# Performance work log

Hardware: AMD Instinct MI355X
Metric: run time of the kernel (lower is better)

The kernel has to match this reference:

```python
import jax, jax.numpy as jnp
import numpy as np

N_NODES = 100000
N_EDGES = 3200000
D_IN = 256
D_OUT = 256


def setup_inputs() -> dict:
    key = jax.random.key(0)
    k1, k2, k3, k4, k5 = jax.random.split(key, 5)
    x = jax.random.normal(k1, (N_NODES, D_IN), dtype=jnp.float32)
    edge_row = jax.random.randint(k2, (N_EDGES,), 0, N_NODES, dtype=jnp.int32)
    edge_col = jax.random.randint(k3, (N_EDGES,), 0, N_NODES, dtype=jnp.int32)
    edge_val = jax.random.uniform(k4, (N_EDGES,), dtype=jnp.float32)
    # Linear weight [out_dim, in_dim], kaiming-uniform-like scale
    bound = 1.0 / np.sqrt(D_IN)
    W = jax.random.uniform(k5, (D_OUT, D_IN), dtype=jnp.float32,
                           minval=-bound, maxval=bound)
    return {"x": x, "edge_row": edge_row, "edge_col": edge_col,
            "edge_val": edge_val, "W": W}


def reference(x, edge_row, edge_col, edge_val, W):
    # SpMM: agg[i] = sum_{edges e with row=i} val_e * x[col_e]
    msgs = edge_val[:, None] * x[edge_col]            # [E, D_IN] gather
    agg = jax.ops.segment_sum(msgs, edge_row, num_segments=N_NODES)  # [N, D_IN]
    # Dense linear projection (bias=False): agg @ W.T
    return agg @ W.T                                  # [N, D_OUT]
```

## Files before the change

kernel.cpp:

```cpp
#include <hip/hip_runtime.h>
#include <stdint.h>

#define N_NODES 100000
#define N_EDGES 3200000
#define D_FEAT 256
#define NBKT 391
#define CHUNK 8192
#define NBLK_E 391

typedef __attribute__((ext_vector_type(8))) short short8;
typedef __attribute__((ext_vector_type(8))) ushort ushort8;
typedef __attribute__((ext_vector_type(4))) float float4v;

__device__ inline unsigned short f2bf(float f) {
    union { float f; unsigned u; } v; v.f = f;
    unsigned u = v.u;
    u += 0x7FFF + ((u >> 16) & 1);
    return (unsigned short)(u >> 16);
}
__device__ inline float bf2f(unsigned short u) {
    union { unsigned u; float f; } v; v.u = (unsigned)u << 16;
    return v.f;
}

__global__ void wconv_kernel(const float* __restrict__ W, ushort* __restrict__ Wbf) {
    int i = blockIdx.x * 256 + threadIdx.x;
    Wbf[i] = f2bf(W[i]);
}

__global__ __launch_bounds__(256) void gemm_x_kernel(
        const float* __restrict__ x,
        const ushort* __restrict__ Wbf,
        ushort* __restrict__ ybf) {
    int w    = threadIdx.x >> 6;
    int lane = threadIdx.x & 63;
    int quad = lane >> 4;
    int l16  = lane & 15;
    int rt   = blockIdx.x * 64;

    float4v acc[4][4];
    #pragma unroll
    for (int mt = 0; mt < 4; ++mt)
        #pragma unroll
        for (int nt = 0; nt < 4; ++nt) acc[mt][nt] = (float4v){0.f, 0.f, 0.f, 0.f};

    #pragma unroll
    for (int k0 = 0; k0 < 256; k0 += 32) {
        short8 a[4], bf[4];
        #pragma unroll
        for (int mt = 0; mt < 4; ++mt) {
            int row = rt + mt * 16 + l16;
            if (row >= N_NODES) row = N_NODES - 1;
            const float4v* p = (const float4v*)&x[(size_t)row * 256 + k0 + quad * 8];
            float4v f0 = p[0], f1 = p[1];
            a[mt][0] = (short)f2bf(f0.x); a[mt][1] = (short)f2bf(f0.y);
            a[mt][2] = (short)f2bf(f0.z); a[mt][3] = (short)f2bf(f0.w);
            a[mt][4] = (short)f2bf(f1.x); a[mt][5] = (short)f2bf(f1.y);
            a[mt][6] = (short)f2bf(f1.z); a[mt][7] = (short)f2bf(f1.w);
        }
        #pragma unroll
        for (int nt = 0; nt < 4; ++nt) {
            int n = w * 64 + nt * 16 + l16;
            bf[nt] = *(const short8*)&Wbf[n * 256 + k0 + quad * 8];
        }
        #pragma unroll
        for (int mt = 0; mt < 4; ++mt)
            #pragma unroll
            for (int nt = 0; nt < 4; ++nt)
                acc[mt][nt] = __builtin_amdgcn_mfma_f32_16x16x32_bf16(a[mt], bf[nt], acc[mt][nt], 0, 0, 0);
    }
    #pragma unroll
    for (int mt = 0; mt < 4; ++mt)
        #pragma unroll
        for (int nt = 0; nt < 4; ++nt) {
            int n = w * 64 + nt * 16 + l16;
            #pragma unroll
            for (int r = 0; r < 4; ++r) {
                int row = rt + mt * 16 + quad * 4 + r;
                if (row < N_NODES) ybf[(size_t)row * 256 + n] = f2bf(acc[mt][nt][r]);
            }
        }
}

__global__ __launch_bounds__(256) void coarse_hist(const int* __restrict__ key,
                                                   int* __restrict__ hist) {
    __shared__ int cnt[NBKT];
    for (int b = threadIdx.x; b < NBKT; b += 256) cnt[b] = 0;
    __syncthreads();
    int cb = blockIdx.x * CHUNK;
    for (int j = 0; j < CHUNK; j += 256) {
        int i = cb + j + threadIdx.x;
        if (i < N_EDGES) atomicAdd(&cnt[key[i] >> 8], 1);
    }
    __syncthreads();
    for (int b = threadIdx.x; b < NBKT; b += 256)
        hist[blockIdx.x * NBKT + b] = cnt[b];
}

__global__ __launch_bounds__(512) void scan_blocks(int* __restrict__ hist,
                                                   int* __restrict__ totals) {
    __shared__ int s[512];
    int b = blockIdx.x;
    int t = threadIdx.x;
    int v = (t < NBLK_E) ? hist[t * NBKT + b] : 0;
    s[t] = v;
    __syncthreads();
    for (int o = 1; o < 512; o <<= 1) {
        int x = (t >= o) ? s[t - o] : 0;
        __syncthreads();
        s[t] += x;
        __syncthreads();
    }
    if (t < NBLK_E) hist[t * NBKT + b] = s[t] - v;
    if (t == NBLK_E - 1) totals[b] = s[t];
}

__global__ __launch_bounds__(512) void scan_buckets(const int* __restrict__ totals,
                                                    int* __restrict__ base_,
                                                    int* __restrict__ row_start) {
    __shared__ int s[512];
    int t = threadIdx.x;
    int v = (t < NBKT) ? totals[t] : 0;
    s[t] = v;
    __syncthreads();
    for (int o = 1; o < 512; o <<= 1) {
        int x = (t >= o) ? s[t - o] : 0;
        __syncthreads();
        s[t] += x;
        __syncthreads();
    }
    if (t < NBKT) base_[t] = s[t] - v;
    if (t == 0) { base_[NBKT] = N_EDGES; row_start[N_NODES] = N_EDGES; }
}

__global__ __launch_bounds__(256) void col_scatter(
        const int* __restrict__ erow, const int* __restrict__ ecol,
        const float* __restrict__ eval,
        const int* __restrict__ hist, const int* __restrict__ base_,
        int* __restrict__ tmpr, uint2* __restrict__ tmpcv) {
    __shared__ int lbase[NBKT];
    __shared__ int cnt[NBKT];
    for (int b = threadIdx.x; b < NBKT; b += 256) {
        lbase[b] = hist[blockIdx.x * NBKT + b] + base_[b];
        cnt[b] = 0;
    }
    __syncthreads();
    int cb = blockIdx.x * CHUNK;
    for (int j = 0; j < CHUNK; j += 256) {
        int i = cb + j + threadIdx.x;
        if (i < N_EDGES) {
            int c = ecol[i];
            int r = erow[i];
            int b = c >> 8;
            int pos = lbase[b] + atomicAdd(&cnt[b], 1);
            tmpr[pos] = r;
            uint2 cv;
            cv.x = (unsigned)c | ((unsigned)(r & 255) << 17);
            union { float f; unsigned u; } w; w.f = eval[i];
            cv.y = w.u;
            tmpcv[pos] = cv;
        }
    }
}

__global__ __launch_bounds__(256) void row_scatter(
        const int* __restrict__ tmpr, const uint2* __restrict__ tmpcv,
        const int* __restrict__ hist, const int* __restrict__ base_,
        uint2* __restrict__ tmp) {
    __shared__ int lbase[NBKT];
    __shared__ int cnt[NBKT];
    for (int b = threadIdx.x; b < NBKT; b += 256) {
        lbase[b] = hist[blockIdx.x * NBKT + b] + base_[b];
        cnt[b] = 0;
    }
    __syncthreads();
    int cb = blockIdx.x * CHUNK;
    for (int j = 0; j < CHUNK; j += 256) {
        int i = cb + j + threadIdx.x;
        if (i < N_EDGES) {
            int b = tmpr[i] >> 8;
            int pos = lbase[b] + atomicAdd(&cnt[b], 1);
            tmp[pos] = tmpcv[i];
        }
    }
}

__global__ __launch_bounds__(256) void fine_sort(const uint2* __restrict__ tmp,
                                                 const int* __restrict__ base_,
                                                 uint2* __restrict__ csr,
                                                 int* __restrict__ row_start) {
    __shared__ int cnt[256];
    __shared__ int excl[256];
    int b = blockIdx.x;
    int t = threadIdx.x;
    int s0 = base_[b];
    int nb = base_[b + 1] - s0;
    cnt[t] = 0;
    __syncthreads();
    for (int j = t; j < nb; j += 256)
        atomicAdd(&cnt[tmp[s0 + j].x >> 17], 1);
    __syncthreads();
    int v = cnt[t];
    excl[t] = v;
    __syncthreads();
    for (int o = 1; o < 256; o <<= 1) {
        int x = (t >= o) ? excl[t - o] : 0;
        __syncthreads();
        excl[t] += x;
        __syncthreads();
    }
    int ex = excl[t] - v;
    int row = b * 256 + t;
    if (row < N_NODES) row_start[row] = s0 + ex;
    excl[t] = ex;
    cnt[t] = 0;
    __syncthreads();
    for (int j = t; j < nb; j += 256) {
        uint2 cv = tmp[s0 + j];
        unsigned rl = cv.x >> 17;
        int dst = s0 + excl[rl] + atomicAdd(&cnt[rl], 1);
        csr[dst] = cv;
    }
}

__global__ __launch_bounds__(256) void spmm_kernel(
        const ushort* __restrict__ ybf,
        const int* __restrict__ row_start,
        const uint2* __restrict__ csr_cv,
        float* __restrict__ out) {
    int row  = (blockIdx.x * blockDim.x + threadIdx.x) >> 6;
    int lane = threadIdx.x & 63;
    int half = lane >> 5;
    int hl   = lane & 31;
    if (row >= N_NODES) return;
    int start = row_start[row];
    int end   = row_start[row + 1];
    float acc[8] = {0.f, 0.f, 0.f, 0.f, 0.f, 0.f, 0.f, 0.f};
    int e = start + half;
    for (; e + 6 < end; e += 8) {
        uint2 cv0 = csr_cv[e];
        uint2 cv1 = csr_cv[e + 2];
        uint2 cv2 = csr_cv[e + 4];
        uint2 cv3 = csr_cv[e + 6];
        ushort8 v0 = *(const ushort8*)&ybf[(size_t)(cv0.x & 0x1FFFF) * 256 + hl * 8];
        ushort8 v1 = *(const ushort8*)&ybf[(size_t)(cv1.x & 0x1FFFF) * 256 + hl * 8];
        ushort8 v2 = *(const ushort8*)&ybf[(size_t)(cv2.x & 0x1FFFF) * 256 + hl * 8];
        ushort8 v3 = *(const ushort8*)&ybf[(size_t)(cv3.x & 0x1FFFF) * 256 + hl * 8];
        union { unsigned u; float f; } w0, w1, w2, w3;
        w0.u = cv0.y; w1.u = cv1.y; w2.u = cv2.y; w3.u = cv3.y;
        #pragma unroll
        for (int j = 0; j < 8; ++j) acc[j] += w0.f * bf2f(v0[j]);
        #pragma unroll
        for (int j = 0; j < 8; ++j) acc[j] += w1.f * bf2f(v1[j]);
        #pragma unroll
        for (int j = 0; j < 8; ++j) acc[j] += w2.f * bf2f(v2[j]);
        #pragma unroll
        for (int j = 0; j < 8; ++j) acc[j] += w3.f * bf2f(v3[j]);
    }
    for (; e < end; e += 2) {
        uint2 cv = csr_cv[e];
        ushort8 v = *(const ushort8*)&ybf[(size_t)(cv.x & 0x1FFFF) * 256 + hl * 8];
        union { unsigned u; float f; } w; w.u = cv.y;
        #pragma unroll
        for (int j = 0; j < 8; ++j) acc[j] += w.f * bf2f(v[j]);
    }
    #pragma unroll
    for (int j = 0; j < 8; ++j) acc[j] += __shfl_xor(acc[j], 32, 64);
    if (half == 0) {
        float4v o0 = {acc[0], acc[1], acc[2], acc[3]};
        float4v o1 = {acc[4], acc[5], acc[6], acc[7]};
        *(float4v*)&out[(size_t)row * 256 + hl * 8]     = o0;
        *(float4v*)&out[(size_t)row * 256 + hl * 8 + 4] = o1;
    }
}


extern "C" void kernel_launch(void* const* d_in, const int* in_sizes, int n_in,
                              void* d_out, int out_size, void* d_ws, size_t ws_size,
                              hipStream_t stream) {
    const float* x    = (const float*)d_in[0];
    const int*   erow = (const int*)d_in[1];
    const int*   ecol = (const int*)d_in[2];
    const float* eval = (const float*)d_in[3];
    const float* W    = (const float*)d_in[4];
    float* out = (float*)d_out;

    char* ws = (char*)d_ws;
    size_t off = 0;
    int* hist      = (int*)(ws + off);   off += ((size_t)NBLK_E * NBKT * 4 + 255) & ~255ull;
    int* totals    = (int*)(ws + off);   off += ((size_t)NBKT * 4 + 255) & ~255ull;
    int* base_     = (int*)(ws + off);   off += ((size_t)(NBKT + 1) * 4 + 255) & ~255ull;
    int* row_start = (int*)(ws + off);   off += ((size_t)(N_NODES + 1) * 4 + 255) & ~255ull;
    int* tmpr      = (int*)(ws + off);   off += ((size_t)N_EDGES * 4 + 255) & ~255ull;
    uint2* tmpcv   = (uint2*)(ws + off); off += (size_t)N_EDGES * 8;
    uint2* tmp_cv  = (uint2*)(ws + off); off += (size_t)N_EDGES * 8;
    uint2* csr_cv  = (uint2*)(ws + off); off += (size_t)N_EDGES * 8;
    ushort* Wbf    = (ushort*)(ws + off);  off += (size_t)D_FEAT * D_FEAT * 2;
    ushort* ybf    = (ushort*)(ws + off);  off += (size_t)N_NODES * D_FEAT * 2;

    wconv_kernel<<<(D_FEAT * D_FEAT) / 256, 256, 0, stream>>>(W, Wbf);
    gemm_x_kernel<<<(N_NODES + 63) / 64, 256, 0, stream>>>(x, Wbf, ybf);

    coarse_hist<<<NBLK_E, 256, 0, stream>>>(ecol, hist);
    scan_blocks<<<NBKT, 512, 0, stream>>>(hist, totals);
    scan_buckets<<<1, 512, 0, stream>>>(totals, base_, row_start);
    col_scatter<<<NBLK_E, 256, 0, stream>>>(erow, ecol, eval, hist, base_, tmpr, tmpcv);
    coarse_hist<<<NBLK_E, 256, 0, stream>>>(tmpr, hist);
    scan_blocks<<<NBKT, 512, 0, stream>>>(hist, totals);
    scan_buckets<<<1, 512, 0, stream>>>(totals, base_, row_start);
    row_scatter<<<NBLK_E, 256, 0, stream>>>(tmpr, tmpcv, hist, base_, tmp_cv);
    fine_sort<<<NBKT, 256, 0, stream>>>(tmp_cv, base_, csr_cv, row_start);

    spmm_kernel<<<N_NODES / 4, 256, 0, stream>>>(ybf, row_start, csr_cv, out);
}
```

Baseline: 701.7 us.

## Replace two-pass radix CSR build with global-atomic row counting and scatter

Drops the column-then-row two-pass bucket sort, with its temporaries and fine-sort pass. It builds the CSR directly: per-row edge counts are taken with global atomics fused into the GEMM kernel, then a two-level scan and a single atomic-cursor scatter follow. This removes several launches and about two full passes over the edge arrays. The catch is that order within a row becomes nondeterministic and the column sort is gone, so gathers from ybf lose locality and global atomics may contend.

```diff
diff --git a/kernel.cpp b/kernel.cpp
--- a/kernel.cpp
+++ b/kernel.cpp
@@ -4,9 +4,8 @@
 #define N_NODES 100000
 #define N_EDGES 3200000
 #define D_FEAT 256
-#define NBKT 391
-#define CHUNK 8192
-#define NBLK_E 391
+#define NROWBLK 391
+#define EPB 2048
 
 typedef __attribute__((ext_vector_type(8))) short short8;
 typedef __attribute__((ext_vector_type(8))) ushort ushort8;
@@ -23,15 +22,32 @@
     return v.f;
 }
 
-__global__ void wconv_kernel(const float* __restrict__ W, ushort* __restrict__ Wbf) {
-    int i = blockIdx.x * 256 + threadIdx.x;
-    Wbf[i] = f2bf(W[i]);
+__global__ __launch_bounds__(256) void prep_kernel(const float* __restrict__ W,
+                                                   ushort* __restrict__ Wbf,
+                                                   int* __restrict__ row_cnt) {
+    int b = blockIdx.x;
+    if (b < 256) {
+        int i = b * 256 + threadIdx.x;
+        Wbf[i] = f2bf(W[i]);
+    } else {
+        int i = (b - 256) * 256 + threadIdx.x;
+        if (i < N_NODES) row_cnt[i] = 0;
+    }
 }
 
 __global__ __launch_bounds__(256) void gemm_x_kernel(
         const float* __restrict__ x,
         const ushort* __restrict__ Wbf,
+        const int* __restrict__ erow,
+        int* __restrict__ row_cnt,
         ushort* __restrict__ ybf) {
+    int eb = blockIdx.x * EPB;
+    #pragma unroll
+    for (int j = 0; j < EPB; j += 256) {
+        int i = eb + j + threadIdx.x;
+        if (i < N_EDGES) atomicAdd(&row_cnt[erow[i]], 1);
+    }
+
     int w    = threadIdx.x >> 6;
     int lane = threadIdx.x & 63;
     int quad = lane >> 4;
@@ -82,37 +98,23 @@
         }
 }
 
-__global__ __launch_bounds__(256) void coarse_hist(const int* __restrict__ key,
-                                                   int* __restrict__ hist) {
-    __shared__ int cnt[NBKT];
-    for (int b = threadIdx.x; b < NBKT; b += 256) cnt[b] = 0;
+__global__ __launch_bounds__(256) void scan_rows(const int* __restrict__ row_cnt,
+                                                 int* __restrict__ row_start,
+                                                 int* __restrict__ totals) {
+    __shared__ int s[256];
+    int b = blockIdx.x, t = threadIdx.x;
+    int row = b * 256 + t;
+    int c = (row < N_NODES) ? row_cnt[row] : 0;
+    s[t] = c;
     __syncthreads();
-    int cb = blockIdx.x * CHUNK;
-    for (int j = 0; j < CHUNK; j += 256) {
-        int i = cb + j + threadIdx.x;
-        if (i < N_EDGES) atomicAdd(&cnt[key[i] >> 8], 1);
-    }
-    __syncthreads();
-    for (int b = threadIdx.x; b < NBKT; b += 256)
-        hist[blockIdx.x * NBKT + b] = cnt[b];
-}
-
-__global__ __launch_bounds__(512) void scan_blocks(int* __restrict__ hist,
-                                                   int* __restrict__ totals) {
-    __shared__ int s[512];
-    int b = blockIdx.x;
-    int t = threadIdx.x;
-    int v = (t < NBLK_E) ? hist[t * NBKT + b] : 0;
-    s[t] = v;
-    __syncthreads();
-    for (int o = 1; o < 512; o <<= 1) {
+    for (int o = 1; o < 256; o <<= 1) {
         int x = (t >= o) ? s[t - o] : 0;
         __syncthreads();
         s[t] += x;
         __syncthreads();
     }
-    if (t < NBLK_E) hist[t * NBKT + b] = s[t] - v;
-    if (t == NBLK_E - 1) totals[b] = s[t];
+    if (row < N_NODES) row_start[row] = s[t] - c;
+    if (t == 255) totals[b] = s[t];
 }
 
 __global__ __launch_bounds__(512) void scan_buckets(const int* __restrict__ totals,
@@ -120,7 +122,7 @@
                                                     int* __restrict__ row_start) {
     __shared__ int s[512];
     int t = threadIdx.x;
-    int v = (t < NBKT) ? totals[t] : 0;
+    int v = (t < NROWBLK) ? totals[t] : 0;
     s[t] = v;
     __syncthreads();
     for (int o = 1; o < 512; o <<= 1) {
@@ -129,98 +131,33 @@
         s[t] += x;
         __syncthreads();
     }
-    if (t < NBKT) base_[t] = s[t] - v;
-    if (t == 0) { base_[NBKT] = N_EDGES; row_start[N_NODES] = N_EDGES; }
-}
-
-__global__ __launch_bounds__(256) void col_scatter(
+    if (t < NROWBLK) base_[t] = s[t] - v;
+    if (t == 0) row_start[N_NODES] = N_EDGES;
+}
+
+__global__ __launch_bounds__(256) void finalize_rows(int* __restrict__ row_start,
+                                                     const int* __restrict__ base_,
+                                                     int* __restrict__ cursor) {
+    int i = blockIdx.x * 256 + threadIdx.x;
+    if (i < N_NODES) {
+        int v = row_start[i] + base_[i >> 8];
+        row_start[i] = v;
+        cursor[i] = v;
+    }
+}
+
+__global__ __launch_bounds__(256) void scatter_kernel(
         const int* __restrict__ erow, const int* __restrict__ ecol,
         const float* __restrict__ eval,
-        const int* __restrict__ hist, const int* __restrict__ base_,
-        int* __restrict__ tmpr, uint2* __restrict__ tmpcv) {
-    __shared__ int lbase[NBKT];
-    __shared__ int cnt[NBKT];
-    for (int b = threadIdx.x; b < NBKT; b += 256) {
-        lbase[b] = hist[blockIdx.x * NBKT + b] + base_[b];
-        cnt[b] = 0;
-    }
-    __syncthreads();
-    int cb = blockIdx.x * CHUNK;
-    for (int j = 0; j < CHUNK; j += 256) {
-        int i = cb + j + threadIdx.x;
-        if (i < N_EDGES) {
-            int c = ecol[i];
-            int r = erow[i];
-            int b = c >> 8;
-            int pos = lbase[b] + atomicAdd(&cnt[b], 1);
-            tmpr[pos] = r;
-            uint2 cv;
-            cv.x = (unsigned)c | ((unsigned)(r & 255) << 17);
-            union { float f; unsigned u; } w; w.f = eval[i];
-            cv.y = w.u;
-            tmpcv[pos] = cv;
-        }
-    }
-}
-
-__global__ __launch_bounds__(256) void row_scatter(
-        const int* __restrict__ tmpr, const uint2* __restrict__ tmpcv,
-        const int* __restrict__ hist, const int* __restrict__ base_,
-        uint2* __restrict__ tmp) {
-    __shared__ int lbase[NBKT];
-    __shared__ int cnt[NBKT];
-    for (int b = threadIdx.x; b < NBKT; b += 256) {
-        lbase[b] = hist[blockIdx.x * NBKT + b] + base_[b];
-        cnt[b] = 0;
-    }
-    __syncthreads();
-    int cb = blockIdx.x * CHUNK;
-    for (int j = 0; j < CHUNK; j += 256) {
-        int i = cb + j + threadIdx.x;
-        if (i < N_EDGES) {
-            int b = tmpr[i] >> 8;
-            int pos = lbase[b] + atomicAdd(&cnt[b], 1);
-            tmp[pos] = tmpcv[i];
-        }
-    }
-}
-
-__global__ __launch_bounds__(256) void fine_sort(const uint2* __restrict__ tmp,
-                                                 const int* __restrict__ base_,
-                                                 uint2* __restrict__ csr,
-                                                 int* __restrict__ row_start) {
-    __shared__ int cnt[256];
-    __shared__ int excl[256];
-    int b = blockIdx.x;
-    int t = threadIdx.x;
-    int s0 = base_[b];
-    int nb = base_[b + 1] - s0;
-    cnt[t] = 0;
-    __syncthreads();
-    for (int j = t; j < nb; j += 256)
-        atomicAdd(&cnt[tmp[s0 + j].x >> 17], 1);
-    __syncthreads();
-    int v = cnt[t];
-    excl[t] = v;
-    __syncthreads();
-    for (int o = 1; o < 256; o <<= 1) {
-        int x = (t >= o) ? excl[t - o] : 0;
-        __syncthreads();
-        excl[t] += x;
-        __syncthreads();
-    }
-    int ex = excl[t] - v;
-    int row = b * 256 + t;
-    if (row < N_NODES) row_start[row] = s0 + ex;
-    excl[t] = ex;
-    cnt[t] = 0;
-    __syncthreads();
-    for (int j = t; j < nb; j += 256) {
-        uint2 cv = tmp[s0 + j];
-        unsigned rl = cv.x >> 17;
-        int dst = s0 + excl[rl] + atomicAdd(&cnt[rl], 1);
-        csr[dst] = cv;
-    }
+        int* __restrict__ cursor, uint2* __restrict__ csr) {
+    int i = blockIdx.x * 256 + threadIdx.x;
+    int r = erow[i];
+    int dst = atomicAdd(&cursor[r], 1);
+    uint2 cv;
+    cv.x = (unsigned)ecol[i];
+    union { float f; unsigned u; } w; w.f = eval[i];
+    cv.y = w.u;
+    csr[dst] = cv;
 }
 
 __global__ __launch_bounds__(256) void spmm_kernel(
@@ -242,10 +179,10 @@
         uint2 cv1 = csr_cv[e + 2];
         uint2 cv2 = csr_cv[e + 4];
         uint2 cv3 = csr_cv[e + 6];
-        ushort8 v0 = *(const ushort8*)&ybf[(size_t)(cv0.x & 0x1FFFF) * 256 + hl * 8];
-        ushort8 v1 = *(const ushort8*)&ybf[(size_t)(cv1.x & 0x1FFFF) * 256 + hl * 8];
-        ushort8 v2 = *(const ushort8*)&ybf[(size_t)(cv2.x & 0x1FFFF) * 256 + hl * 8];
-        ushort8 v3 = *(const ushort8*)&ybf[(size_t)(cv3.x & 0x1FFFF) * 256 + hl * 8];
+        ushort8 v0 = *(const ushort8*)&ybf[(size_t)cv0.x * 256 + hl * 8];
+        ushort8 v1 = *(const ushort8*)&ybf[(size_t)cv1.x * 256 + hl * 8];
+        ushort8 v2 = *(const ushort8*)&ybf[(size_t)cv2.x * 256 + hl * 8];
+        ushort8 v3 = *(const ushort8*)&ybf[(size_t)cv3.x * 256 + hl * 8];
         union { unsigned u; float f; } w0, w1, w2, w3;
         w0.u = cv0.y; w1.u = cv1.y; w2.u = cv2.y; w3.u = cv3.y;
         #pragma unroll
@@ -259,7 +196,7 @@
     }
     for (; e < end; e += 2) {
         uint2 cv = csr_cv[e];
-        ushort8 v = *(const ushort8*)&ybf[(size_t)(cv.x & 0x1FFFF) * 256 + hl * 8];
+        ushort8 v = *(const ushort8*)&ybf[(size_t)cv.x * 256 + hl * 8];
         union { unsigned u; float f; } w; w.u = cv.y;
         #pragma unroll
         for (int j = 0; j < 8; ++j) acc[j] += w.f * bf2f(v[j]);
@@ -287,29 +224,20 @@
 
     char* ws = (char*)d_ws;
     size_t off = 0;
-    int* hist      = (int*)(ws + off);   off += ((size_t)NBLK_E * NBKT * 4 + 255) & ~255ull;
-    int* totals    = (int*)(ws + off);   off += ((size_t)NBKT * 4 + 255) & ~255ull;
-    int* base_     = (int*)(ws + off);   off += ((size_t)(NBKT + 1) * 4 + 255) & ~255ull;
+    int* row_cnt   = (int*)(ws + off);   off += ((size_t)N_NODES * 4 + 255) & ~255ull;
     int* row_start = (int*)(ws + off);   off += ((size_t)(N_NODES + 1) * 4 + 255) & ~255ull;
-    int* tmpr      = (int*)(ws + off);   off += ((size_t)N_EDGES * 4 + 255) & ~255ull;
-    uint2* tmpcv   = (uint2*)(ws + off); off += (size_t)N_EDGES * 8;
-    uint2* tmp_cv  = (uint2*)(ws + off); off += (size_t)N_EDGES * 8;
+    int* cursor    = (int*)(ws + off);   off += ((size_t)N_NODES * 4 + 255) & ~255ull;
+    int* totals    = (int*)(ws + off);   off += ((size_t)NROWBLK * 4 + 255) & ~255ull;
+    int* base_     = (int*)(ws + off);   off += ((size_t)NROWBLK * 4 + 255) & ~255ull;
     uint2* csr_cv  = (uint2*)(ws + off); off += (size_t)N_EDGES * 8;
     ushort* Wbf    = (ushort*)(ws + off);  off += (size_t)D_FEAT * D_FEAT * 2;
     ushort* ybf    = (ushort*)(ws + off);  off += (size_t)N_NODES * D_FEAT * 2;
 
-    wconv_kernel<<<(D_FEAT * D_FEAT) / 256, 256, 0, stream>>>(W, Wbf);
-    gemm_x_kernel<<<(N_NODES + 63) / 64, 256, 0, stream>>>(x, Wbf, ybf);
-
-    coarse_hist<<<NBLK_E, 256, 0, stream>>>(ecol, hist);
-    scan_blocks<<<NBKT, 512, 0, stream>>>(hist, totals);
+    prep_kernel<<<256 + NROWBLK, 256, 0, stream>>>(W, Wbf, row_cnt);
+    gemm_x_kernel<<<(N_NODES + 63) / 64, 256, 0, stream>>>(x, Wbf, erow, row_cnt, ybf);
+    scan_rows<<<NROWBLK, 256, 0, stream>>>(row_cnt, row_start, totals);
     scan_buckets<<<1, 512, 0, stream>>>(totals, base_, row_start);
-    col_scatter<<<NBLK_E, 256, 0, stream>>>(erow, ecol, eval, hist, base_, tmpr, tmpcv);
-    coarse_hist<<<NBLK_E, 256, 0, stream>>>(tmpr, hist);
-    scan_blocks<<<NBKT, 512, 0, stream>>>(hist, totals);
-    scan_buckets<<<1, 512, 0, stream>>>(totals, base_, row_start);
-    row_scatter<<<NBLK_E, 256, 0, stream>>>(tmpr, tmpcv, hist, base_, tmp_cv);
-    fine_sort<<<NBKT, 256, 0, stream>>>(tmp_cv, base_, csr_cv, row_start);
-
+    finalize_rows<<<NROWBLK, 256, 0, stream>>>(row_start, base_, cursor);
+    scatter_kernel<<<N_EDGES / 256, 256, 0, stream>>>(erow, ecol, eval, cursor, csr_cv);
     spmm_kernel<<<N_NODES / 4, 256, 0, stream>>>(ybf, row_start, csr_cv, out);
 }
```

After: 828.3 us. 1.18x slower.

## Replace column-then-row bucket sort with two-level row radix partitioning

Applied to the files above, without the earlier changes.

The sort pipeline changes from a column-bucket pass followed by a row-bucket pass to an MSD-style two-level partition on the row key. The first level uses 25 coarse buckets (row>>12), the second uses 391 buckets (row>>8). The intermediate row key is stored as a 16-bit value instead of a 32-bit int, which cuts scatter traffic. Edges within a row are no longer pre-ordered by column, so x-row gather locality in the SpMM may drop. The coarse first scatter with only 25 buckets also risks more contention on the shared-memory atomics.

```diff
diff --git a/kernel.cpp b/kernel.cpp
--- a/kernel.cpp
+++ b/kernel.cpp
@@ -4,9 +4,10 @@
 #define N_NODES 100000
 #define N_EDGES 3200000
 #define D_FEAT 256
-#define NBKT 391
 #define CHUNK 8192
 #define NBLK_E 391
+#define NB1 25
+#define NB2 391
 
 typedef __attribute__((ext_vector_type(8))) short short8;
 typedef __attribute__((ext_vector_type(8))) ushort ushort8;
@@ -82,27 +83,42 @@
         }
 }
 
-__global__ __launch_bounds__(256) void coarse_hist(const int* __restrict__ key,
-                                                   int* __restrict__ hist) {
-    __shared__ int cnt[NBKT];
-    for (int b = threadIdx.x; b < NBKT; b += 256) cnt[b] = 0;
+__global__ __launch_bounds__(256) void hist1_kernel(const int* __restrict__ erow,
+                                                    int* __restrict__ hist) {
+    __shared__ int cnt[NB1];
+    if (threadIdx.x < NB1) cnt[threadIdx.x] = 0;
     __syncthreads();
     int cb = blockIdx.x * CHUNK;
     for (int j = 0; j < CHUNK; j += 256) {
         int i = cb + j + threadIdx.x;
-        if (i < N_EDGES) atomicAdd(&cnt[key[i] >> 8], 1);
-    }
-    __syncthreads();
-    for (int b = threadIdx.x; b < NBKT; b += 256)
-        hist[blockIdx.x * NBKT + b] = cnt[b];
+        if (i < N_EDGES) atomicAdd(&cnt[erow[i] >> 12], 1);
+    }
+    __syncthreads();
+    if (threadIdx.x < NB1) hist[blockIdx.x * NB1 + threadIdx.x] = cnt[threadIdx.x];
+}
+
+__global__ __launch_bounds__(256) void hist2_kernel(const ushort* __restrict__ rh1,
+                                                    int* __restrict__ hist) {
+    __shared__ int cnt[NB2];
+    for (int b = threadIdx.x; b < NB2; b += 256) cnt[b] = 0;
+    __syncthreads();
+    int cb = blockIdx.x * CHUNK;
+    for (int j = 0; j < CHUNK; j += 256) {
+        int i = cb + j + threadIdx.x;
+        if (i < N_EDGES) atomicAdd(&cnt[rh1[i]], 1);
+    }
+    __syncthreads();
+    for (int b = threadIdx.x; b < NB2; b += 256)
+        hist[blockIdx.x * NB2 + b] = cnt[b];
 }
 
 __global__ __launch_bounds__(512) void scan_blocks(int* __restrict__ hist,
-                                                   int* __restrict__ totals) {
+                                                   int* __restrict__ totals,
+                                                   int nbkt) {
     __shared__ int s[512];
     int b = blockIdx.x;
     int t = threadIdx.x;
-    int v = (t < NBLK_E) ? hist[t * NBKT + b] : 0;
+    int v = (t < NBLK_E) ? hist[t * nbkt + b] : 0;
     s[t] = v;
     __syncthreads();
     for (int o = 1; o < 512; o <<= 1) {
@@ -111,16 +127,16 @@
         s[t] += x;
         __syncthreads();
     }
-    if (t < NBLK_E) hist[t * NBKT + b] = s[t] - v;
+    if (t < NBLK_E) hist[t * nbkt + b] = s[t] - v;
     if (t == NBLK_E - 1) totals[b] = s[t];
 }
 
 __global__ __launch_bounds__(512) void scan_buckets(const int* __restrict__ totals,
                                                     int* __restrict__ base_,
-                                                    int* __restrict__ row_start) {
+                                                    int n, int* __restrict__ row_start) {
     __shared__ int s[512];
     int t = threadIdx.x;
-    int v = (t < NBKT) ? totals[t] : 0;
+    int v = (t < n) ? totals[t] : 0;
     s[t] = v;
     __syncthreads();
     for (int o = 1; o < 512; o <<= 1) {
@@ -129,19 +145,51 @@
         s[t] += x;
         __syncthreads();
     }
-    if (t < NBKT) base_[t] = s[t] - v;
-    if (t == 0) { base_[NBKT] = N_EDGES; row_start[N_NODES] = N_EDGES; }
-}
-
-__global__ __launch_bounds__(256) void col_scatter(
+    if (t < n) base_[t] = s[t] - v;
+    if (t == 0) {
+        base_[n] = N_EDGES;
+        if (row_start) row_start[N_NODES] = N_EDGES;
+    }
+}
+
+__global__ __launch_bounds__(256) void scatter1_kernel(
         const int* __restrict__ erow, const int* __restrict__ ecol,
         const float* __restrict__ eval,
-        const int* __restrict__ hist, const int* __restrict__ base_,
-        int* __restrict__ tmpr, uint2* __restrict__ tmpcv) {
-    __shared__ int lbase[NBKT];
-    __shared__ int cnt[NBKT];
-    for (int b = threadIdx.x; b < NBKT; b += 256) {
-        lbase[b] = hist[blockIdx.x * NBKT + b] + base_[b];
+        const int* __restrict__ hist1, const int* __restrict__ base1,
+        ushort* __restrict__ rh1, uint2* __restrict__ cv1) {
+    __shared__ int lbase[NB1];
+    __shared__ int cnt[NB1];
+    int t = threadIdx.x;
+    if (t < NB1) {
+        lbase[t] = hist1[blockIdx.x * NB1 + t] + base1[t];
+        cnt[t] = 0;
+    }
+    __syncthreads();
+    int cb = blockIdx.x * CHUNK;
+    for (int j = 0; j < CHUNK; j += 256) {
+        int i = cb + j + t;
+        if (i < N_EDGES) {
+            int r = erow[i];
+            int b = r >> 12;
+            int pos = lbase[b] + atomicAdd(&cnt[b], 1);
+            rh1[pos] = (unsigned short)(r >> 8);
+            uint2 cv;
+            cv.x = (unsigned)ecol[i] | ((unsigned)(r & 255) << 17);
+            union { float f; unsigned u; } w; w.f = eval[i];
+            cv.y = w.u;
+            cv1[pos] = cv;
+        }
+    }
+}
+
+__global__ __launch_bounds__(256) void scatter2_kernel(
+        const ushort* __restrict__ rh1, const uint2* __restrict__ cv1,
+        const int* __restrict__ hist2, const int* __restrict__ base2,
+        uint2* __restrict__ tmp2) {
+    __shared__ int lbase[NB2];
+    __shared__ int cnt[NB2];
+    for (int b = threadIdx.x; b < NB2; b += 256) {
+        lbase[b] = hist2[blockIdx.x * NB2 + b] + base2[b];
         cnt[b] = 0;
     }
     __syncthreads();
@@ -149,38 +197,9 @@
     for (int j = 0; j < CHUNK; j += 256) {
         int i = cb + j + threadIdx.x;
         if (i < N_EDGES) {
-            int c = ecol[i];
-            int r = erow[i];
-            int b = c >> 8;
+            int b = rh1[i];
             int pos = lbase[b] + atomicAdd(&cnt[b], 1);
-            tmpr[pos] = r;
-            uint2 cv;
-            cv.x = (unsigned)c | ((unsigned)(r & 255) << 17);
-            union { float f; unsigned u; } w; w.f = eval[i];
-            cv.y = w.u;
-            tmpcv[pos] = cv;
-        }
-    }
-}
-
-__global__ __launch_bounds__(256) void row_scatter(
-        const int* __restrict__ tmpr, const uint2* __restrict__ tmpcv,
-        const int* __restrict__ hist, const int* __restrict__ base_,
-        uint2* __restrict__ tmp) {
-    __shared__ int lbase[NBKT];
-    __shared__ int cnt[NBKT];
-    for (int b = threadIdx.x; b < NBKT; b += 256) {
-        lbase[b] = hist[blockIdx.x * NBKT + b] + base_[b];
-        cnt[b] = 0;
-    }
-    __syncthreads();
-    int cb = blockIdx.x * CHUNK;
-    for (int j = 0; j < CHUNK; j += 256) {
-        int i = cb + j + threadIdx.x;
-        if (i < N_EDGES) {
-            int b = tmpr[i] >> 8;
-            int pos = lbase[b] + atomicAdd(&cnt[b], 1);
-            tmp[pos] = tmpcv[i];
+            tmp2[pos] = cv1[i];
         }
     }
 }
@@ -287,29 +306,32 @@
 
     char* ws = (char*)d_ws;
     size_t off = 0;
-    int* hist      = (int*)(ws + off);   off += ((size_t)NBLK_E * NBKT * 4 + 255) & ~255ull;
-    int* totals    = (int*)(ws + off);   off += ((size_t)NBKT * 4 + 255) & ~255ull;
-    int* base_     = (int*)(ws + off);   off += ((size_t)(NBKT + 1) * 4 + 255) & ~255ull;
+    int* hist1     = (int*)(ws + off);   off += ((size_t)NBLK_E * NB1 * 4 + 255) & ~255ull;
+    int* hist2     = (int*)(ws + off);   off += ((size_t)NBLK_E * NB2 * 4 + 255) & ~255ull;
+    int* totals1   = (int*)(ws + off);   off += (512 * 4);
+    int* base1     = (int*)(ws + off);   off += (512 * 4);
+    int* totals2   = (int*)(ws + off);   off += (512 * 4);
+    int* base2     = (int*)(ws + off);   off += (512 * 4);
     int* row_start = (int*)(ws + off);   off += ((size_t)(N_NODES + 1) * 4 + 255) & ~255ull;
-    int* tmpr      = (int*)(ws + off);   off += ((size_t)N_EDGES * 4 + 255) & ~255ull;
-    uint2* tmpcv   = (uint2*)(ws + off); off += (size_t)N_EDGES * 8;
-    uint2* tmp_cv  = (uint2*)(ws + off); off += (size_t)N_EDGES * 8;
-    uint2* csr_cv  = (uint2*)(ws + off); off += (size_t)N_EDGES * 8;
-    ushort* Wbf    = (ushort*)(ws + off);  off += (size_t)D_FEAT * D_FEAT * 2;
-    ushort* ybf    = (ushort*)(ws + off);  off += (size_t)N_NODES * D_FEAT * 2;
+    ushort* rh1    = (ushort*)(ws + off); off += ((size_t)N_EDGES * 2 + 255) & ~255ull;
+    uint2* cv1     = (uint2*)(ws + off);  off += (size_t)N_EDGES * 8;
+    uint2* tmp2    = (uint2*)(ws + off);  off += (size_t)N_EDGES * 8;
+    uint2* csr_cv  = (uint2*)(ws + off);  off += (size_t)N_EDGES * 8;
+    ushort* Wbf    = (ushort*)(ws + off); off += (size_t)D_FEAT * D_FEAT * 2;
+    ushort* ybf    = (ushort*)(ws + off); off += (size_t)N_NODES * D_FEAT * 2;
 
     wconv_kernel<<<(D_FEAT * D_FEAT) / 256, 256, 0, stream>>>(W, Wbf);
     gemm_x_kernel<<<(N_NODES + 63) / 64, 256, 0, stream>>>(x, Wbf, ybf);
 
-    coarse_hist<<<NBLK_E, 256, 0, stream>>>(ecol, hist);
-    scan_blocks<<<NBKT, 512, 0, stream>>>(hist, totals);
-    scan_buckets<<<1, 512, 0, stream>>>(totals, base_, row_start);
-    col_scatter<<<NBLK_E, 256, 0, stream>>>(erow, ecol, eval, hist, base_, tmpr, tmpcv);
-    coarse_hist<<<NBLK_E, 256, 0, stream>>>(tmpr, hist);
-    scan_blocks<<<NBKT, 512, 0, stream>>>(hist, totals);
-    scan_buckets<<<1, 512, 0, stream>>>(totals, base_, row_start);
-    row_scatter<<<NBLK_E, 256, 0, stream>>>(tmpr, tmpcv, hist, base_, tmp_cv);
-    fine_sort<<<NBKT, 256, 0, stream>>>(tmp_cv, base_, csr_cv, row_start);
+    hist1_kernel<<<NBLK_E, 256, 0, stream>>>(erow, hist1);
+    scan_blocks<<<NB1, 512, 0, stream>>>(hist1, totals1, NB1);
+    scan_buckets<<<1, 512, 0, stream>>>(totals1, base1, NB1, nullptr);
+    scatter1_kernel<<<NBLK_E, 256, 0, stream>>>(erow, ecol, eval, hist1, base1, rh1, cv1);
+    hist2_kernel<<<NBLK_E, 256, 0, stream>>>(rh1, hist2);
+    scan_blocks<<<NB2, 512, 0, stream>>>(hist2, totals2, NB2);
+    scan_buckets<<<1, 512, 0, stream>>>(totals2, base2, NB2, row_start);
+    scatter2_kernel<<<NBLK_E, 256, 0, stream>>>(rh1, cv1, hist2, base2, tmp2);
+    fine_sort<<<NB2, 256, 0, stream>>>(tmp2, base2, csr_cv, row_start);
 
     spmm_kernel<<<N_NODES / 4, 256, 0, stream>>>(ybf, row_start, csr_cv, out);
 }
```

Measured after the change: 615.4 us. 1.14x faster.

## Drop column pre-sort pass; bucket edges by row directly with wider blocks

Applied to the files above, without the earlier changes.

Removes the first sort pass that ordered edges by column bucket, along with its histogram, scans and temporary arrays. Edges now go straight into row buckets in a single scatter, then the fine sort runs as before. Histogram and scatter blocks grow to 1024 threads and fine_sort to 512 threads. Within each row the edges lose their column-sorted order, so gathers in the SpMM may have worse cache locality, and the fine sort's atomic order makes summation order nondeterministic.

```diff
diff --git a/kernel.cpp b/kernel.cpp
--- a/kernel.cpp
+++ b/kernel.cpp
@@ -4,9 +4,10 @@
 #define N_NODES 100000
 #define N_EDGES 3200000
 #define D_FEAT 256
-#define NBKT 391
 #define CHUNK 8192
 #define NBLK_E 391
+#define NBKT 391
+#define CT 1024
 
 typedef __attribute__((ext_vector_type(8))) short short8;
 typedef __attribute__((ext_vector_type(8))) ushort ushort8;
@@ -82,19 +83,19 @@
         }
 }
 
-__global__ __launch_bounds__(256) void coarse_hist(const int* __restrict__ key,
-                                                   int* __restrict__ hist) {
+__global__ __launch_bounds__(CT) void hist_kernel(const int* __restrict__ erow,
+                                                  int* __restrict__ hist) {
     __shared__ int cnt[NBKT];
-    for (int b = threadIdx.x; b < NBKT; b += 256) cnt[b] = 0;
+    if (threadIdx.x < NBKT) cnt[threadIdx.x] = 0;
     __syncthreads();
     int cb = blockIdx.x * CHUNK;
-    for (int j = 0; j < CHUNK; j += 256) {
+    #pragma unroll
+    for (int j = 0; j < CHUNK; j += CT) {
         int i = cb + j + threadIdx.x;
-        if (i < N_EDGES) atomicAdd(&cnt[key[i] >> 8], 1);
-    }
-    __syncthreads();
-    for (int b = threadIdx.x; b < NBKT; b += 256)
-        hist[blockIdx.x * NBKT + b] = cnt[b];
+        if (i < N_EDGES) atomicAdd(&cnt[erow[i] >> 8], 1);
+    }
+    __syncthreads();
+    if (threadIdx.x < NBKT) hist[blockIdx.x * NBKT + threadIdx.x] = cnt[threadIdx.x];
 }
 
 __global__ __launch_bounds__(512) void scan_blocks(int* __restrict__ hist,
@@ -133,59 +134,37 @@
     if (t == 0) { base_[NBKT] = N_EDGES; row_start[N_NODES] = N_EDGES; }
 }
 
-__global__ __launch_bounds__(256) void col_scatter(
+__global__ __launch_bounds__(CT) void scatter_kernel(
         const int* __restrict__ erow, const int* __restrict__ ecol,
         const float* __restrict__ eval,
-        const int* __restrict__ hist, const int* __restrict__ base_,
-        int* __restrict__ tmpr, uint2* __restrict__ tmpcv) {
-    __shared__ int lbase[NBKT];
-    __shared__ int cnt[NBKT];
-    for (int b = threadIdx.x; b < NBKT; b += 256) {
-        lbase[b] = hist[blockIdx.x * NBKT + b] + base_[b];
-        cnt[b] = 0;
-    }
-    __syncthreads();
-    int cb = blockIdx.x * CHUNK;
-    for (int j = 0; j < CHUNK; j += 256) {
-        int i = cb + j + threadIdx.x;
-        if (i < N_EDGES) {
-            int c = ecol[i];
-            int r = erow[i];
-            int b = c >> 8;
-            int pos = lbase[b] + atomicAdd(&cnt[b], 1);
-            tmpr[pos] = r;
-            uint2 cv;
-            cv.x = (unsigned)c | ((unsigned)(r & 255) << 17);
-            union { float f; unsigned u; } w; w.f = eval[i];
-            cv.y = w.u;
-            tmpcv[pos] = cv;
-        }
-    }
-}
-
-__global__ __launch_bounds__(256) void row_scatter(
-        const int* __restrict__ tmpr, const uint2* __restrict__ tmpcv,
         const int* __restrict__ hist, const int* __restrict__ base_,
         uint2* __restrict__ tmp) {
     __shared__ int lbase[NBKT];
     __shared__ int cnt[NBKT];
-    for (int b = threadIdx.x; b < NBKT; b += 256) {
-        lbase[b] = hist[blockIdx.x * NBKT + b] + base_[b];
-        cnt[b] = 0;
+    int t = threadIdx.x;
+    if (t < NBKT) {
+        lbase[t] = hist[blockIdx.x * NBKT + t] + base_[t];
+        cnt[t] = 0;
     }
     __syncthreads();
     int cb = blockIdx.x * CHUNK;
-    for (int j = 0; j < CHUNK; j += 256) {
-        int i = cb + j + threadIdx.x;
+    #pragma unroll
+    for (int j = 0; j < CHUNK; j += CT) {
+        int i = cb + j + t;
         if (i < N_EDGES) {
-            int b = tmpr[i] >> 8;
+            int r = erow[i];
+            int b = r >> 8;
             int pos = lbase[b] + atomicAdd(&cnt[b], 1);
-            tmp[pos] = tmpcv[i];
-        }
-    }
-}
-
-__global__ __launch_bounds__(256) void fine_sort(const uint2* __restrict__ tmp,
+            uint2 cv;
+            cv.x = (unsigned)ecol[i] | ((unsigned)(r & 255) << 17);
+            union { float f; unsigned u; } w; w.f = eval[i];
+            cv.y = w.u;
+            tmp[pos] = cv;
+        }
+    }
+}
+
+__global__ __launch_bounds__(512) void fine_sort(const uint2* __restrict__ tmp,
                                                  const int* __restrict__ base_,
                                                  uint2* __restrict__ csr,
                                                  int* __restrict__ row_start) {
@@ -195,27 +174,30 @@
     int t = threadIdx.x;
     int s0 = base_[b];
     int nb = base_[b + 1] - s0;
-    cnt[t] = 0;
-    __syncthreads();
-    for (int j = t; j < nb; j += 256)
+    if (t < 256) cnt[t] = 0;
+    __syncthreads();
+    for (int j = t; j < nb; j += 512)
         atomicAdd(&cnt[tmp[s0 + j].x >> 17], 1);
     __syncthreads();
-    int v = cnt[t];
-    excl[t] = v;
+    int v = 0;
+    if (t < 256) { v = cnt[t]; excl[t] = v; }
     __syncthreads();
     for (int o = 1; o < 256; o <<= 1) {
-        int x = (t >= o) ? excl[t - o] : 0;
-        __syncthreads();
-        excl[t] += x;
-        __syncthreads();
-    }
-    int ex = excl[t] - v;
-    int row = b * 256 + t;
-    if (row < N_NODES) row_start[row] = s0 + ex;
-    excl[t] = ex;
-    cnt[t] = 0;
-    __syncthreads();
-    for (int j = t; j < nb; j += 256) {
+        int x = 0;
+        if (t >= o && t < 256) x = excl[t - o];
+        __syncthreads();
+        if (t < 256) excl[t] += x;
+        __syncthreads();
+    }
+    if (t < 256) {
+        int ex = excl[t] - v;
+        int row = b * 256 + t;
+        if (row < N_NODES) row_start[row] = s0 + ex;
+        excl[t] = ex;
+        cnt[t] = 0;
+    }
+    __syncthreads();
+    for (int j = t; j < nb; j += 512) {
         uint2 cv = tmp[s0 + j];
         unsigned rl = cv.x >> 17;
         int dst = s0 + excl[rl] + atomicAdd(&cnt[rl], 1);
@@ -288,28 +270,22 @@
     char* ws = (char*)d_ws;
     size_t off = 0;
     int* hist      = (int*)(ws + off);   off += ((size_t)NBLK_E * NBKT * 4 + 255) & ~255ull;
-    int* totals    = (int*)(ws + off);   off += ((size_t)NBKT * 4 + 255) & ~255ull;
+    int* totals    = (int*)(ws + off);   off += (512 * 4);
     int* base_     = (int*)(ws + off);   off += ((size_t)(NBKT + 1) * 4 + 255) & ~255ull;
     int* row_start = (int*)(ws + off);   off += ((size_t)(N_NODES + 1) * 4 + 255) & ~255ull;
-    int* tmpr      = (int*)(ws + off);   off += ((size_t)N_EDGES * 4 + 255) & ~255ull;
-    uint2* tmpcv   = (uint2*)(ws + off); off += (size_t)N_EDGES * 8;
-    uint2* tmp_cv  = (uint2*)(ws + off); off += (size_t)N_EDGES * 8;
-    uint2* csr_cv  = (uint2*)(ws + off); off += (size_t)N_EDGES * 8;
-    ushort* Wbf    = (ushort*)(ws + off);  off += (size_t)D_FEAT * D_FEAT * 2;
-    ushort* ybf    = (ushort*)(ws + off);  off += (size_t)N_NODES * D_FEAT * 2;
+    uint2* tmp     = (uint2*)(ws + off); off += (size_t)N_EDGES * 8;
+    uint2* csr     = (uint2*)(ws + off); off += (size_t)N_EDGES * 8;
+    ushort* Wbf    = (ushort*)(ws + off); off += (size_t)D_FEAT * D_FEAT * 2;
+    ushort* ybf    = (ushort*)(ws + off); off += (size_t)N_NODES * D_FEAT * 2;
 
     wconv_kernel<<<(D_FEAT * D_FEAT) / 256, 256, 0, stream>>>(W, Wbf);
     gemm_x_kernel<<<(N_NODES + 63) / 64, 256, 0, stream>>>(x, Wbf, ybf);
 
-    coarse_hist<<<NBLK_E, 256, 0, stream>>>(ecol, hist);
+    hist_kernel<<<NBLK_E, CT, 0, stream>>>(erow, hist);
     scan_blocks<<<NBKT, 512, 0, stream>>>(hist, totals);
     scan_buckets<<<1, 512, 0, stream>>>(totals, base_, row_start);
-    col_scatter<<<NBLK_E, 256, 0, stream>>>(erow, ecol, eval, hist, base_, tmpr, tmpcv);
-    coarse_hist<<<NBLK_E, 256, 0, stream>>>(tmpr, hist);
-    scan_blocks<<<NBKT, 512, 0, stream>>>(hist, totals);
-    scan_buckets<<<1, 512, 0, stream>>>(totals, base_, row_start);
-    row_scatter<<<NBLK_E, 256, 0, stream>>>(tmpr, tmpcv, hist, base_, tmp_cv);
-    fine_sort<<<NBKT, 256, 0, stream>>>(tmp_cv, base_, csr_cv, row_start);
-
-    spmm_kernel<<<N_NODES / 4, 256, 0, stream>>>(ybf, row_start, csr_cv, out);
-}
+    scatter_kernel<<<NBLK_E, CT, 0, stream>>>(erow, ecol, eval, hist, base_, tmp);
+    fine_sort<<<NBKT, 512, 0, stream>>>(tmp, base_, csr, row_start);
+
+    spmm_kernel<<<N_NODES / 4, 256, 0, stream>>>(ybf, row_start, csr, out);
+}
```

Result: faster. 570.2 us (-18.7%).
